# Optimization experiments

Hardware: AMD Instinct MI355X
Metric: run time of the kernel (lower is better)

## Reference

```python
import jax, jax.numpy as jnp
import numpy as np

TOP_K = 2


def setup_inputs() -> dict:
    key = jax.random.key(0)
    ks = jax.random.split(key, 8)
    B, S, H, I, E = 1, 1024, 2048, 1408, 8
    s = 0.02  # init scale for weights
    return {
        "hidden_states": jax.random.normal(ks[0], (B, S, H), jnp.float32),
        "gate_weight": jax.random.normal(ks[1], (E, H), jnp.float32) * s,
        "expert_gate_w": jax.random.normal(ks[2], (E, I, H), jnp.float32) * s,
        "expert_up_w": jax.random.normal(ks[3], (E, I, H), jnp.float32) * s,
        "expert_down_w": jax.random.normal(ks[4], (E, H, I), jnp.float32) * s,
        "shared_gate_w": jax.random.normal(ks[5], (I, H), jnp.float32) * s,
        "shared_up_w": jax.random.normal(ks[6], (I, H), jnp.float32) * s,
        "shared_down_w": jax.random.normal(ks[7], (H, I), jnp.float32) * s,
    }


def reference(hidden_states, gate_weight, expert_gate_w, expert_up_w, expert_down_w,
              shared_gate_w, shared_up_w, shared_down_w):
    B, S, H = hidden_states.shape
    E = gate_weight.shape[0]
    x = hidden_states.reshape(-1, H)          # [T, H]
    T = x.shape[0]

    # --- gate: top-k routing (e_score_correction_bias buffer is zeros -> no-op) ---
    logits = x @ gate_weight.T                # [T, E]
    topk_logits, topk_idx = jax.lax.top_k(logits, TOP_K)
    topk_w = jax.nn.softmax(topk_logits, axis=-1)  # [T, K]

    # per-token per-expert combine weight (0 for non-selected experts) [T, E]
    comb = jnp.zeros((T, E), x.dtype).at[jnp.arange(T)[:, None], topk_idx].add(topk_w)

    # --- routed experts: dense over E, weighted combine (mathematically identical
    # to the per-token loop since comb==0 for unselected experts) ---
    g = jnp.einsum('th,eih->tei', x, expert_gate_w)   # [T, E, I]
    u = jnp.einsum('th,eih->tei', x, expert_up_w)     # [T, E, I]
    h = jax.nn.silu(g) * u                            # [T, E, I]
    y = jnp.einsum('tei,ehi->teh', h, expert_down_w)  # [T, E, H]
    out = jnp.einsum('teh,te->th', y, comb)           # [T, H]

    # --- shared expert ---
    sh = (jax.nn.silu(x @ shared_gate_w.T) * (x @ shared_up_w.T)) @ shared_down_w.T
    out = out + sh
    return out.reshape(B, S, H)
```

## Files before the change

kernel.cpp:

```cpp
#include <hip/hip_runtime.h>
#include <hip/hip_bf16.h>

typedef unsigned short u16;
typedef __bf16 bf16x8 __attribute__((ext_vector_type(8)));
typedef float f32x4 __attribute__((ext_vector_type(4)));

#define H_DIM 2048
#define I_DIM 1408
#define T_TOK 1024
#define NEXP 8
#define LS 40

__device__ __forceinline__ u16 f2bf(float f) {
    union { float f; unsigned u; } v; v.f = f;
    unsigned r = v.u + 0x7FFFu + ((v.u >> 16) & 1u);
    return (u16)(r >> 16);
}
__device__ __forceinline__ unsigned pack2(float a, float b) {
    float2 t; t.x = a; t.y = b;
    __hip_bfloat162 h = __float22bfloat162_rn(t);
    union { __hip_bfloat162 h; unsigned u; } v; v.h = h;
    return v.u;
}
__device__ __forceinline__ uint2 pack4(float4 f) {
    uint2 r; r.x = pack2(f.x, f.y); r.y = pack2(f.z, f.w); return r;
}
__device__ __forceinline__ void g2l16(const void* g, void* l) {
    __builtin_amdgcn_global_load_lds((const __attribute__((address_space(1))) void*)g,
                                     (__attribute__((address_space(3))) void*)l, 16, 0, 0);
}

struct PrepArgs {
    const float* cin[6]; u16* cout[6]; int n16[6];
    const float* x; const float* gw; u16* xb;
    int* counts; int* tok; float* tw; unsigned* tslot;
};

__global__ __launch_bounds__(256)
void prep_kernel(PrepArgs a) {
    int z = blockIdx.z;
    if (z < 6) {
        int n = a.n16[z];
        const float4* in = (const float4*)a.cin[z];
        uint4* out = (uint4*)a.cout[z];
        for (int i = blockIdx.x * 256 + threadIdx.x; i < n; i += gridDim.x * 256) {
            const float4* p = in + (size_t)i * 4;
            float4 f0 = p[0], f1 = p[1], f2 = p[2], f3 = p[3];
            uint4 o0, o1;
            o0.x = pack2(f0.x, f0.y); o0.y = pack2(f0.z, f0.w);
            o0.z = pack2(f1.x, f1.y); o0.w = pack2(f1.z, f1.w);
            o1.x = pack2(f2.x, f2.y); o1.y = pack2(f2.z, f2.w);
            o1.z = pack2(f3.x, f3.y); o1.w = pack2(f3.z, f3.w);
            out[(size_t)i * 2]     = o0;
            out[(size_t)i * 2 + 1] = o1;
        }
    } else {
        if (blockIdx.x >= 256) return;
        int wave = threadIdx.x >> 6, lane = threadIdx.x & 63;
        int t = blockIdx.x * 4 + wave;
        const float4* xr = (const float4*)(a.x + (size_t)t * H_DIM);
        const float4* gw4 = (const float4*)a.gw;
        uint2* xbr = (uint2*)(a.xb + (size_t)t * H_DIM);
        float acc[NEXP];
#pragma unroll
        for (int e = 0; e < NEXP; e++) acc[e] = 0.f;
#pragma unroll
        for (int j = 0; j < 8; j++) {
            int c = lane + j * 64;
            float4 xv = xr[c];
            xbr[c] = pack4(xv);
#pragma unroll
            for (int e = 0; e < NEXP; e++) {
                float4 gv = gw4[e * 512 + c];
                acc[e] += xv.x * gv.x + xv.y * gv.y + xv.z * gv.z + xv.w * gv.w;
            }
        }
#pragma unroll
        for (int e = 0; e < NEXP; e++) {
#pragma unroll
            for (int off = 32; off > 0; off >>= 1) acc[e] += __shfl_xor(acc[e], off);
        }
        if (lane == 0) {
            int i0 = 0; float v0 = acc[0];
#pragma unroll
            for (int e = 1; e < NEXP; e++) if (acc[e] > v0) { v0 = acc[e]; i0 = e; }
            int i1 = -1; float v1 = -3.0e38f;
#pragma unroll
            for (int e = 0; e < NEXP; e++) if (e != i0 && acc[e] > v1) { v1 = acc[e]; i1 = e; }
            float ex = __expf(v1 - v0);
            float w0 = 1.f / (1.f + ex);
            float w1 = 1.f - w0;
            int s0 = atomicAdd(&a.counts[i0], 1);
            a.tok[i0 * T_TOK + s0] = t; a.tw[i0 * T_TOK + s0] = w0;
            a.tslot[t * 2] = ((unsigned)i0 << 16) | (unsigned)s0;
            int s1 = atomicAdd(&a.counts[i1], 1);
            a.tok[i1 * T_TOK + s1] = t; a.tw[i1 * T_TOK + s1] = w1;
            a.tslot[t * 2 + 1] = ((unsigned)i1 << 16) | (unsigned)s1;
        }
    }
}

__global__ __launch_bounds__(128, 2)
void gate_up_bf(const u16* __restrict__ xb,
                const u16* __restrict__ egb, const u16* __restrict__ eub,
                const u16* __restrict__ sgb, const u16* __restrict__ sub,
                const int* __restrict__ counts, const int* __restrict__ tok,
                const float* __restrict__ tw,
                u16* __restrict__ h_r, u16* __restrict__ h_s) {
    __shared__ u16 lA[64 * 64];
    __shared__ u16 lG[128 * 64];
    __shared__ u16 lU[128 * 64];

    int e = blockIdx.z;
    bool routed = (e < NEXP);
    int cnt, hbase; const u16 *Wg, *Wu; u16* hout;
    if (routed) {
        cnt = counts[e];
        int p = 0;
#pragma unroll
        for (int i = 0; i < NEXP; i++) { int c = counts[i]; if (i < e) p += c; }
        hbase = p;
        Wg = egb + (size_t)e * I_DIM * H_DIM;
        Wu = eub + (size_t)e * I_DIM * H_DIM;
        hout = h_r;
    } else { cnt = T_TOK; hbase = 0; Wg = sgb; Wu = sub; hout = h_s; }
    int m0 = blockIdx.y * 64;
    if (m0 >= cnt) return;
    int n0 = blockIdx.x * 128;

    int tid = threadIdx.x, lane = tid & 63, w = tid >> 6;
    int l3 = lane >> 3, cl = lane & 7;
    int cg = cl ^ l3;

    const u16* aptr[4];
#pragma unroll
    for (int j = 0; j < 4; j++) {
        int row = w * 32 + j * 8 + l3;
        int trow = m0 + row; if (trow > cnt - 1) trow = cnt - 1;
        int tix = routed ? tok[e * T_TOK + trow] : trow;
        aptr[j] = xb + (size_t)tix * H_DIM + cg * 8;
    }
    const u16* gbase = Wg + (size_t)(n0 + w * 64 + l3) * H_DIM + cg * 8;
    const u16* ubase = Wu + (size_t)(n0 + w * 64 + l3) * H_DIM + cg * 8;

    u16* aldsb = &lA[w * 2048];
    u16* gldsb = &lG[w * 4096];
    u16* uldsb = &lU[w * 4096];

    f32x4 zero = {0.f, 0.f, 0.f, 0.f};
    f32x4 accg[4][4], accu[4][4];
#pragma unroll
    for (int a = 0; a < 4; a++)
#pragma unroll
        for (int b = 0; b < 4; b++) { accg[a][b] = zero; accu[a][b] = zero; }

    int r16 = lane & 15, q = lane >> 4;

    for (int k0 = 0; k0 < H_DIM; k0 += 64) {
#pragma unroll
        for (int j = 0; j < 4; j++) g2l16(aptr[j] + k0, aldsb + j * 512);
#pragma unroll
        for (int j = 0; j < 8; j++) {
            g2l16(gbase + (size_t)j * 8 * H_DIM + k0, gldsb + j * 512);
            g2l16(ubase + (size_t)j * 8 * H_DIM + k0, uldsb + j * 512);
        }
        __syncthreads();
#pragma unroll
        for (int kh = 0; kh < 2; kh++) {
            bf16x8 af[4], gf[4], uf[4];
#pragma unroll
            for (int mi = 0; mi < 4; mi++) {
                int row = mi * 16 + r16;
                int ch = (kh * 4 + q) ^ (row & 7);
                af[mi] = *(const bf16x8*)&lA[row * 64 + ch * 8];
            }
#pragma unroll
            for (int ni = 0; ni < 4; ni++) {
                int row = w * 64 + ni * 16 + r16;
                int ch = (kh * 4 + q) ^ (row & 7);
                gf[ni] = *(const bf16x8*)&lG[row * 64 + ch * 8];
                uf[ni] = *(const bf16x8*)&lU[row * 64 + ch * 8];
            }
#pragma unroll
            for (int mi = 0; mi < 4; mi++)
#pragma unroll
                for (int ni = 0; ni < 4; ni++) {
                    accg[mi][ni] = __builtin_amdgcn_mfma_f32_16x16x32_bf16(af[mi], gf[ni], accg[mi][ni], 0, 0, 0);
                    accu[mi][ni] = __builtin_amdgcn_mfma_f32_16x16x32_bf16(af[mi], uf[ni], accu[mi][ni], 0, 0, 0);
                }
        }
        __syncthreads();
    }

#pragma unroll
    for (int mi = 0; mi < 4; mi++) {
#pragma unroll
        for (int r = 0; r < 4; r++) {
            int row = mi * 16 + q * 4 + r;
            int gr = m0 + row;
            if (gr < cnt) {
                float wt = routed ? tw[e * T_TOK + gr] : 1.0f;
                u16* hrow = hout + (size_t)(hbase + gr) * I_DIM + n0 + w * 64;
#pragma unroll
                for (int ni = 0; ni < 4; ni++) {
                    float g = accg[mi][ni][r], u = accu[mi][ni][r];
                    hrow[ni * 16 + r16] = f2bf((g / (1.f + __expf(-g))) * u * wt);
                }
            }
        }
    }
}

__global__ __launch_bounds__(128, 2)
void down_bf(const u16* __restrict__ h_r, const u16* __restrict__ h_s,
             const u16* __restrict__ edb, const u16* __restrict__ sdb,
             const int* __restrict__ counts, const int* __restrict__ tok,
             float* __restrict__ y_r, float* __restrict__ y_s) {
    __shared__ u16 lA[64 * 64];
    __shared__ u16 lB[128 * 64];

    int e = blockIdx.z;
    bool routed = (e < NEXP);
    int cnt, hbase; const u16* Wd; const u16* hin;
    if (routed) {
        cnt = counts[e];
        int p = 0;
#pragma unroll
        for (int i = 0; i < NEXP; i++) { int c = counts[i]; if (i < e) p += c; }
        hbase = p;
        Wd = edb + (size_t)e * H_DIM * I_DIM;
        hin = h_r;
    } else { cnt = T_TOK; hbase = 0; Wd = sdb; hin = h_s; }
    int m0 = blockIdx.y * 64;
    if (m0 >= cnt) return;
    int n0 = blockIdx.x * 128;

    int tid = threadIdx.x, lane = tid & 63, w = tid >> 6;
    int l3 = lane >> 3, cl = lane & 7;
    int cg = cl ^ l3;

    const u16* aptr[4];
#pragma unroll
    for (int j = 0; j < 4; j++) {
        int row = w * 32 + j * 8 + l3;
        int hr = m0 + row; if (hr > cnt - 1) hr = cnt - 1;
        aptr[j] = hin + (size_t)(hbase + hr) * I_DIM + cg * 8;
    }
    const u16* bbase = Wd + (size_t)(n0 + w * 64 + l3) * I_DIM + cg * 8;

    u16* aldsb = &lA[w * 2048];
    u16* bldsb = &lB[w * 4096];

    f32x4 zero = {0.f, 0.f, 0.f, 0.f};
    f32x4 acc[4][4];
#pragma unroll
    for (int a = 0; a < 4; a++)
#pragma unroll
        for (int b = 0; b < 4; b++) acc[a][b] = zero;

    int r16 = lane & 15, q = lane >> 4;

    for (int k0 = 0; k0 < I_DIM; k0 += 64) {
#pragma unroll
        for (int j = 0; j < 4; j++) g2l16(aptr[j] + k0, aldsb + j * 512);
#pragma unroll
        for (int j = 0; j < 8; j++) g2l16(bbase + (size_t)j * 8 * I_DIM + k0, bldsb + j * 512);
        __syncthreads();
#pragma unroll
        for (int kh = 0; kh < 2; kh++) {
            bf16x8 af[4], bfr[4];
#pragma unroll
            for (int mi = 0; mi < 4; mi++) {
                int row = mi * 16 + r16;
                int ch = (kh * 4 + q) ^ (row & 7);
                af[mi] = *(const bf16x8*)&lA[row * 64 + ch * 8];
            }
#pragma unroll
            for (int ni = 0; ni < 4; ni++) {
                int row = w * 64 + ni * 16 + r16;
                int ch = (kh * 4 + q) ^ (row & 7);
                bfr[ni] = *(const bf16x8*)&lB[row * 64 + ch * 8];
            }
#pragma unroll
            for (int mi = 0; mi < 4; mi++)
#pragma unroll
                for (int ni = 0; ni < 4; ni++)
                    acc[mi][ni] = __builtin_amdgcn_mfma_f32_16x16x32_bf16(af[mi], bfr[ni], acc[mi][ni], 0, 0, 0);
        }
        __syncthreads();
    }

#pragma unroll
    for (int mi = 0; mi < 4; mi++) {
#pragma unroll
        for (int r = 0; r < 4; r++) {
            int row = mi * 16 + q * 4 + r;
            int gr = m0 + row;
            if (gr < cnt) {
                float* yrow = (routed ? y_r + (size_t)(hbase + gr) * H_DIM
                                      : y_s + (size_t)gr * H_DIM) + n0 + w * 64;
#pragma unroll
                for (int ni = 0; ni < 4; ni++)
                    yrow[ni * 16 + r16] = acc[mi][ni][r];
            }
        }
    }
}

__global__ __launch_bounds__(256)
void reduce_kernel(const int* __restrict__ counts, const unsigned* __restrict__ tslot,
                   const float* __restrict__ y_r, const float* __restrict__ y_s,
                   float* __restrict__ out) {
    int t = blockIdx.x;
    int pre[NEXP]; int run = 0;
#pragma unroll
    for (int i = 0; i < NEXP; i++) { pre[i] = run; run += counts[i]; }
    unsigned t0 = tslot[t * 2], t1 = tslot[t * 2 + 1];
    int r0 = pre[t0 >> 16] + (int)(t0 & 0xffffu);
    int r1 = pre[t1 >> 16] + (int)(t1 & 0xffffu);
    const float4* ys = (const float4*)(y_s + (size_t)t * H_DIM);
    const float4* a0 = (const float4*)(y_r + (size_t)r0 * H_DIM);
    const float4* a1 = (const float4*)(y_r + (size_t)r1 * H_DIM);
    float4* o = (float4*)(out + (size_t)t * H_DIM);
#pragma unroll
    for (int j = 0; j < 2; j++) {
        int c = threadIdx.x + j * 256;
        float4 s = ys[c], b0 = a0[c], b1 = a1[c];
        float4 r;
        r.x = s.x + b0.x + b1.x; r.y = s.y + b0.y + b1.y;
        r.z = s.z + b0.z + b1.z; r.w = s.w + b0.w + b1.w;
        o[c] = r;
    }
}

__global__ __launch_bounds__(256)
void router_kernel(const float* __restrict__ x, const float* __restrict__ gw,
                   int* __restrict__ counts, int* __restrict__ tok, float* __restrict__ tw) {
    int wave = threadIdx.x >> 6;
    int lane = threadIdx.x & 63;
    int t = blockIdx.x * 4 + wave;
    const float* xr = x + (size_t)t * H_DIM;
    float acc[NEXP];
#pragma unroll
    for (int e = 0; e < NEXP; e++) acc[e] = 0.f;
    for (int h = lane; h < H_DIM; h += 64) {
        float xv = xr[h];
#pragma unroll
        for (int e = 0; e < NEXP; e++) acc[e] += xv * gw[e * H_DIM + h];
    }
#pragma unroll
    for (int e = 0; e < NEXP; e++) {
#pragma unroll
        for (int off = 32; off > 0; off >>= 1) acc[e] += __shfl_xor(acc[e], off);
    }
    if (lane == 0) {
        int i0 = 0; float v0 = acc[0];
#pragma unroll
        for (int e = 1; e < NEXP; e++) if (acc[e] > v0) { v0 = acc[e]; i0 = e; }
        int i1 = -1; float v1 = -3.0e38f;
#pragma unroll
        for (int e = 0; e < NEXP; e++) if (e != i0 && acc[e] > v1) { v1 = acc[e]; i1 = e; }
        float ex = __expf(v1 - v0);
        float w0 = 1.f / (1.f + ex);
        float w1 = 1.f - w0;
        int s0 = atomicAdd(&counts[i0], 1);
        tok[i0 * T_TOK + s0] = t; tw[i0 * T_TOK + s0] = w0;
        int s1 = atomicAdd(&counts[i1], 1);
        tok[i1 * T_TOK + s1] = t; tw[i1 * T_TOK + s1] = w1;
    }
}

__global__ __launch_bounds__(256, 2)
void gate_up_f32(const float* __restrict__ x,
                 const float* __restrict__ egw, const float* __restrict__ euw,
                 const float* __restrict__ sgw, const float* __restrict__ suw,
                 const int* __restrict__ counts, const int* __restrict__ tok,
                 const float* __restrict__ tw,
                 u16* __restrict__ h_r, u16* __restrict__ h_s) {
    __shared__ u16 lA[64 * LS];
    __shared__ u16 lG[128 * LS];
    __shared__ u16 lU[128 * LS];
    int e = blockIdx.z;
    bool routed = (e < NEXP);
    int cnt, hbase; const float *Wg, *Wu; u16* hout;
    if (routed) {
// ... 114 lines not shown
    int hr = m0 + arow; if (hr > cnt - 1) hr = cnt - 1;
    const u16* ap = hin + (size_t)(hbase + hr) * I_DIM + ac8 * 8;
    int sa = arow * LS + ac8 * 8;
    const float* bp[4]; int sb[4];
#pragma unroll
    for (int i = 0; i < 4; i++) {
        int slot = tid + i * 256;
        int row = slot >> 3, c4 = slot & 7;
        bp[i] = Wd + (size_t)(n0 + row) * I_DIM + c4 * 4;
        sb[i] = row * LS + c4 * 4;
    }
    f32x4 zero = {0.f, 0.f, 0.f, 0.f};
    f32x4 acc[4][2];
#pragma unroll
    for (int a = 0; a < 4; a++)
#pragma unroll
        for (int b = 0; b < 2; b++) acc[a][b] = zero;
    int r16 = lane & 15, kq = lane >> 4;
    uint4 ra = *(const uint4*)(ap);
    float4 rb[4];
#pragma unroll
    for (int i = 0; i < 4; i++) rb[i] = *(const float4*)(bp[i]);
    for (int k0 = 0; k0 < I_DIM; k0 += 32) {
        *(uint4*)&lA[sa] = ra;
#pragma unroll
        for (int i = 0; i < 4; i++) *(uint2*)&lB[sb[i]] = pack4(rb[i]);
        __syncthreads();
        if (k0 + 32 < I_DIM) {
            int kn = k0 + 32;
            ra = *(const uint4*)(ap + kn);
#pragma unroll
            for (int i = 0; i < 4; i++) rb[i] = *(const float4*)(bp[i] + kn);
        }
        bf16x8 af[4], bfr[2];
#pragma unroll
        for (int mi = 0; mi < 4; mi++) af[mi] = *(const bf16x8*)&lA[(mi * 16 + r16) * LS + kq * 8];
#pragma unroll
        for (int ni = 0; ni < 2; ni++) bfr[ni] = *(const bf16x8*)&lB[(w * 32 + ni * 16 + r16) * LS + kq * 8];
#pragma unroll
        for (int mi = 0; mi < 4; mi++)
#pragma unroll
            for (int ni = 0; ni < 2; ni++)
                acc[mi][ni] = __builtin_amdgcn_mfma_f32_16x16x32_bf16(af[mi], bfr[ni], acc[mi][ni], 0, 0, 0);
        __syncthreads();
    }
#pragma unroll
    for (int mi = 0; mi < 4; mi++) {
#pragma unroll
        for (int r = 0; r < 4; r++) {
            int row = mi * 16 + kq * 4 + r;
            int gr = m0 + row;
            if (gr < cnt) {
                int t = routed ? tok[e * T_TOK + gr] : gr;
                float* orow = out + (size_t)t * H_DIM + n0 + w * 32;
#pragma unroll
                for (int ni = 0; ni < 2; ni++)
                    atomicAdd(&orow[ni * 16 + r16], acc[mi][ni][r]);
            }
        }
    }
}

extern "C" void kernel_launch(void* const* d_in, const int* in_sizes, int n_in,
                              void* d_out, int out_size, void* d_ws, size_t ws_size,
                              hipStream_t stream) {
    const float* x   = (const float*)d_in[0];
    const float* gw  = (const float*)d_in[1];
    const float* egw = (const float*)d_in[2];
    const float* euw = (const float*)d_in[3];
    const float* edw = (const float*)d_in[4];
    const float* sgw = (const float*)d_in[5];
    const float* suw = (const float*)d_in[6];
    const float* sdw = (const float*)d_in[7];
    float* out = (float*)d_out;

    char* ws = (char*)d_ws;
    int*      counts = (int*)ws;
    int*      tok    = (int*)(ws + 256);
    float*    tw     = (float*)(ws + 33024);
    unsigned* tslot  = (unsigned*)(ws + 65792);
    u16*      h_r    = (u16*)(ws + 73984);
    u16*      h_s    = (u16*)(ws + 5841152);
    u16*      xb     = (u16*)(ws + 8724736);
    u16*      egb    = (u16*)(ws + 12919040);
    u16*      eub    = (u16*)(ws + 59056384);
    u16*      edb    = (u16*)(ws + 105193728);
    u16*      sgb    = (u16*)(ws + 151331072);
    u16*      sub    = (u16*)(ws + 157098240);
    u16*      sdb    = (u16*)(ws + 162865408);
    float*    y_r    = (float*)(ws + 12919040);
    float*    y_s    = (float*)(ws + 29696256);

    hipMemsetAsync(counts, 0, 32, stream);

    const size_t NEED = 168632576ull;
    if (ws_size >= NEED) {
        PrepArgs pa;
        pa.cin[0] = egw; pa.cout[0] = egb; pa.n16[0] = 1441792;
        pa.cin[1] = euw; pa.cout[1] = eub; pa.n16[1] = 1441792;
        pa.cin[2] = edw; pa.cout[2] = edb; pa.n16[2] = 1441792;
        pa.cin[3] = sgw; pa.cout[3] = sgb; pa.n16[3] = 180224;
        pa.cin[4] = suw; pa.cout[4] = sub; pa.n16[4] = 180224;
        pa.cin[5] = sdw; pa.cout[5] = sdb; pa.n16[5] = 180224;
        pa.x = x; pa.gw = gw; pa.xb = xb;
        pa.counts = counts; pa.tok = tok; pa.tw = tw; pa.tslot = tslot;
        prep_kernel<<<dim3(1024, 1, 7), 256, 0, stream>>>(pa);
        gate_up_bf<<<dim3(11, 16, 9), 128, 0, stream>>>(xb, egb, eub, sgb, sub, counts, tok, tw, h_r, h_s);
        down_bf<<<dim3(16, 16, 9), 128, 0, stream>>>(h_r, h_s, edb, sdb, counts, tok, y_r, y_s);
        reduce_kernel<<<1024, 256, 0, stream>>>(counts, tslot, y_r, y_s, out);
    } else {
        hipMemsetAsync(out, 0, (size_t)T_TOK * H_DIM * sizeof(float), stream);
        router_kernel<<<256, 256, 0, stream>>>(x, gw, counts, tok, tw);
        gate_up_f32<<<dim3(11, 16, 9), 256, 0, stream>>>(x, egw, euw, sgw, suw, counts, tok, tw, h_r, h_s);
        down_f32<<<dim3(16, 16, 9), 256, 0, stream>>>(h_r, h_s, edw, sdw, counts, tok, out);
    }
}
```

Before: 504.0 us.

## Overlap down-weight bf16 conversion with gate/up GEMM and use 4-wave blocks

The fp32-to-bf16 conversion of the down-projection weights moves out of the prep kernel into an extra z-slice of the gate/up GEMM launch, so it runs alongside the GEMM blocks. The prep kernel now converts only the gate/up weights, using a flat block mapping and batched loads. Both GEMM kernels switch from 2 waves to 4 waves per block with a 64x128 tile, so each wave now owns a 32-column slice, and launch bounds target 3 blocks per CU. This is meant to hide conversion bandwidth behind compute and raise occupancy, at the cost of fewer MFMAs per LDS fragment load.

```diff
diff --git a/kernel.cpp b/kernel.cpp
--- a/kernel.cpp
+++ b/kernel.cpp
@@ -30,34 +30,35 @@
                                      (__attribute__((address_space(3))) void*)l, 16, 0, 0);
 }
 
-struct PrepArgs {
-    const float* cin[6]; u16* cout[6]; int n16[6];
+struct Prep1Args {
+    const float* src[4]; u16* dst[4];
     const float* x; const float* gw; u16* xb;
     int* counts; int* tok; float* tw; unsigned* tslot;
 };
 
 __global__ __launch_bounds__(256)
-void prep_kernel(PrepArgs a) {
-    int z = blockIdx.z;
-    if (z < 6) {
-        int n = a.n16[z];
-        const float4* in = (const float4*)a.cin[z];
-        uint4* out = (uint4*)a.cout[z];
-        for (int i = blockIdx.x * 256 + threadIdx.x; i < n; i += gridDim.x * 256) {
-            const float4* p = in + (size_t)i * 4;
-            float4 f0 = p[0], f1 = p[1], f2 = p[2], f3 = p[3];
-            uint4 o0, o1;
-            o0.x = pack2(f0.x, f0.y); o0.y = pack2(f0.z, f0.w);
-            o0.z = pack2(f1.x, f1.y); o0.w = pack2(f1.z, f1.w);
-            o1.x = pack2(f2.x, f2.y); o1.y = pack2(f2.z, f2.w);
-            o1.z = pack2(f3.x, f3.y); o1.w = pack2(f3.z, f3.w);
-            out[(size_t)i * 2]     = o0;
-            out[(size_t)i * 2 + 1] = o1;
+void prep1_kernel(Prep1Args a) {
+    int b = blockIdx.x;
+    if (b < 1584) {
+        int r, rb;
+        if (b < 704)       { r = 0; rb = b; }
+        else if (b < 1408) { r = 1; rb = b - 704; }
+        else if (b < 1496) { r = 2; rb = b - 1408; }
+        else               { r = 3; rb = b - 1496; }
+        const float4* in = (const float4*)a.src[r];
+        uint2* out = (uint2*)a.dst[r];
+        size_t base = (size_t)rb * 8192 + threadIdx.x;
+#pragma unroll
+        for (int it = 0; it < 4; it++) {
+            float4 v[8];
+#pragma unroll
+            for (int j = 0; j < 8; j++) v[j] = in[base + it * 2048 + j * 256];
+#pragma unroll
+            for (int j = 0; j < 8; j++) out[base + it * 2048 + j * 256] = pack4(v[j]);
         }
     } else {
-        if (blockIdx.x >= 256) return;
         int wave = threadIdx.x >> 6, lane = threadIdx.x & 63;
-        int t = blockIdx.x * 4 + wave;
+        int t = (b - 1584) * 4 + wave;
         const float4* xr = (const float4*)(a.x + (size_t)t * H_DIM);
         const float4* gw4 = (const float4*)a.gw;
         uint2* xbr = (uint2*)(a.xb + (size_t)t * H_DIM);
@@ -100,18 +101,46 @@
     }
 }
 
-__global__ __launch_bounds__(128, 2)
+#define EDW_F4 5767168
+__global__ __launch_bounds__(256, 3)
 void gate_up_bf(const u16* __restrict__ xb,
                 const u16* __restrict__ egb, const u16* __restrict__ eub,
                 const u16* __restrict__ sgb, const u16* __restrict__ sub,
                 const int* __restrict__ counts, const int* __restrict__ tok,
                 const float* __restrict__ tw,
-                u16* __restrict__ h_r, u16* __restrict__ h_s) {
+                u16* __restrict__ h_r, u16* __restrict__ h_s,
+                const float* __restrict__ edw_f, const float* __restrict__ sdw_f,
+                u16* __restrict__ edb, u16* __restrict__ sdb) {
+    int e = blockIdx.z;
+    if (e == 9) {
+        int b = blockIdx.y * 11 + blockIdx.x;
+        size_t base = (size_t)b * 36864 + threadIdx.x;
+        const float4* ein = (const float4*)edw_f;
+        const float4* sin_ = (const float4*)sdw_f;
+        uint2* eout = (uint2*)edb;
+        uint2* sout = (uint2*)sdb;
+        for (int it = 0; it < 18; it++) {
+            size_t g0 = base + (size_t)it * 2048;
+            float4 v[8];
+#pragma unroll
+            for (int j = 0; j < 8; j++) {
+                size_t g = g0 + j * 256;
+                v[j] = (g < EDW_F4) ? ein[g] : sin_[g - EDW_F4];
+            }
+#pragma unroll
+            for (int j = 0; j < 8; j++) {
+                size_t g = g0 + j * 256;
+                if (g < EDW_F4) eout[g] = pack4(v[j]);
+                else            sout[g - EDW_F4] = pack4(v[j]);
+            }
+        }
+        return;
+    }
+
     __shared__ u16 lA[64 * 64];
     __shared__ u16 lG[128 * 64];
     __shared__ u16 lU[128 * 64];
 
-    int e = blockIdx.z;
     bool routed = (e < NEXP);
     int cnt, hbase; const u16 *Wg, *Wu; u16* hout;
     if (routed) {
@@ -129,45 +158,48 @@
     int n0 = blockIdx.x * 128;
 
     int tid = threadIdx.x, lane = tid & 63, w = tid >> 6;
-    int l3 = lane >> 3, cl = lane & 7;
-    int cg = cl ^ l3;
-
-    const u16* aptr[4];
-#pragma unroll
-    for (int j = 0; j < 4; j++) {
-        int row = w * 32 + j * 8 + l3;
+
+    const u16* aptr[2]; u16* alds[2];
+#pragma unroll
+    for (int j = 0; j < 2; j++) {
+        int chunk = w * 128 + j * 64 + lane;
+        int row = chunk >> 3, cl = chunk & 7;
+        int cg = cl ^ (row & 7);
         int trow = m0 + row; if (trow > cnt - 1) trow = cnt - 1;
         int tix = routed ? tok[e * T_TOK + trow] : trow;
         aptr[j] = xb + (size_t)tix * H_DIM + cg * 8;
-    }
-    const u16* gbase = Wg + (size_t)(n0 + w * 64 + l3) * H_DIM + cg * 8;
-    const u16* ubase = Wu + (size_t)(n0 + w * 64 + l3) * H_DIM + cg * 8;
-
-    u16* aldsb = &lA[w * 2048];
-    u16* gldsb = &lG[w * 4096];
-    u16* uldsb = &lU[w * 4096];
+        alds[j] = &lA[(w * 128 + j * 64) * 8];
+    }
+    const u16* gptr[4]; const u16* uptr[4]; u16* glds[4]; u16* ulds[4];
+#pragma unroll
+    for (int j = 0; j < 4; j++) {
+        int chunk = w * 256 + j * 64 + lane;
+        int row = chunk >> 3, cl = chunk & 7;
+        int cg = cl ^ (row & 7);
+        gptr[j] = Wg + (size_t)(n0 + row) * H_DIM + cg * 8;
+        uptr[j] = Wu + (size_t)(n0 + row) * H_DIM + cg * 8;
+        glds[j] = &lG[(w * 256 + j * 64) * 8];
+        ulds[j] = &lU[(w * 256 + j * 64) * 8];
+    }
 
     f32x4 zero = {0.f, 0.f, 0.f, 0.f};
-    f32x4 accg[4][4], accu[4][4];
+    f32x4 accg[4][2], accu[4][2];
 #pragma unroll
     for (int a = 0; a < 4; a++)
 #pragma unroll
-        for (int b = 0; b < 4; b++) { accg[a][b] = zero; accu[a][b] = zero; }
+        for (int b = 0; b < 2; b++) { accg[a][b] = zero; accu[a][b] = zero; }
 
     int r16 = lane & 15, q = lane >> 4;
 
     for (int k0 = 0; k0 < H_DIM; k0 += 64) {
 #pragma unroll
-        for (int j = 0; j < 4; j++) g2l16(aptr[j] + k0, aldsb + j * 512);
-#pragma unroll
-        for (int j = 0; j < 8; j++) {
-            g2l16(gbase + (size_t)j * 8 * H_DIM + k0, gldsb + j * 512);
-            g2l16(ubase + (size_t)j * 8 * H_DIM + k0, uldsb + j * 512);
-        }
+        for (int j = 0; j < 2; j++) g2l16(aptr[j] + k0, alds[j]);
+#pragma unroll
+        for (int j = 0; j < 4; j++) { g2l16(gptr[j] + k0, glds[j]); g2l16(uptr[j] + k0, ulds[j]); }
         __syncthreads();
 #pragma unroll
         for (int kh = 0; kh < 2; kh++) {
-            bf16x8 af[4], gf[4], uf[4];
+            bf16x8 af[4], gf[2], uf[2];
 #pragma unroll
             for (int mi = 0; mi < 4; mi++) {
                 int row = mi * 16 + r16;
@@ -175,8 +207,8 @@
                 af[mi] = *(const bf16x8*)&lA[row * 64 + ch * 8];
             }
 #pragma unroll
-            for (int ni = 0; ni < 4; ni++) {
-                int row = w * 64 + ni * 16 + r16;
+            for (int ni = 0; ni < 2; ni++) {
+                int row = w * 32 + ni * 16 + r16;
                 int ch = (kh * 4 + q) ^ (row & 7);
                 gf[ni] = *(const bf16x8*)&lG[row * 64 + ch * 8];
                 uf[ni] = *(const bf16x8*)&lU[row * 64 + ch * 8];
@@ -184,7 +216,7 @@
 #pragma unroll
             for (int mi = 0; mi < 4; mi++)
 #pragma unroll
-                for (int ni = 0; ni < 4; ni++) {
+                for (int ni = 0; ni < 2; ni++) {
                     accg[mi][ni] = __builtin_amdgcn_mfma_f32_16x16x32_bf16(af[mi], gf[ni], accg[mi][ni], 0, 0, 0);
                     accu[mi][ni] = __builtin_amdgcn_mfma_f32_16x16x32_bf16(af[mi], uf[ni], accu[mi][ni], 0, 0, 0);
                 }
@@ -200,9 +232,9 @@
             int gr = m0 + row;
             if (gr < cnt) {
                 float wt = routed ? tw[e * T_TOK + gr] : 1.0f;
-                u16* hrow = hout + (size_t)(hbase + gr) * I_DIM + n0 + w * 64;
-#pragma unroll
-                for (int ni = 0; ni < 4; ni++) {
+                u16* hrow = hout + (size_t)(hbase + gr) * I_DIM + n0 + w * 32;
+#pragma unroll
+                for (int ni = 0; ni < 2; ni++) {
                     float g = accg[mi][ni][r], u = accu[mi][ni][r];
                     hrow[ni * 16 + r16] = f2bf((g / (1.f + __expf(-g))) * u * wt);
                 }
@@ -211,7 +243,7 @@
     }
 }
 
-__global__ __launch_bounds__(128, 2)
+__global__ __launch_bounds__(256, 3)
 void down_bf(const u16* __restrict__ h_r, const u16* __restrict__ h_s,
              const u16* __restrict__ edb, const u16* __restrict__ sdb,
              const int* __restrict__ counts, const int* __restrict__ tok,
@@ -236,39 +268,45 @@
     int n0 = blockIdx.x * 128;
 
     int tid = threadIdx.x, lane = tid & 63, w = tid >> 6;
-    int l3 = lane >> 3, cl = lane & 7;
-    int cg = cl ^ l3;
-
-    const u16* aptr[4];
-#pragma unroll
-    for (int j = 0; j < 4; j++) {
-        int row = w * 32 + j * 8 + l3;
+
+    const u16* aptr[2]; u16* alds[2];
+#pragma unroll
+    for (int j = 0; j < 2; j++) {
+        int chunk = w * 128 + j * 64 + lane;
+        int row = chunk >> 3, cl = chunk & 7;
+        int cg = cl ^ (row & 7);
         int hr = m0 + row; if (hr > cnt - 1) hr = cnt - 1;
         aptr[j] = hin + (size_t)(hbase + hr) * I_DIM + cg * 8;
-    }
-    const u16* bbase = Wd + (size_t)(n0 + w * 64 + l3) * I_DIM + cg * 8;
-
-    u16* aldsb = &lA[w * 2048];
-    u16* bldsb = &lB[w * 4096];
+        alds[j] = &lA[(w * 128 + j * 64) * 8];
+    }
+    const u16* bptr[4]; u16* blds[4];
+#pragma unroll
+    for (int j = 0; j < 4; j++) {
+        int chunk = w * 256 + j * 64 + lane;
+        int row = chunk >> 3, cl = chunk & 7;
+        int cg = cl ^ (row & 7);
+        bptr[j] = Wd + (size_t)(n0 + row) * I_DIM + cg * 8;
+        blds[j] = &lB[(w * 256 + j * 64) * 8];
+    }
 
     f32x4 zero = {0.f, 0.f, 0.f, 0.f};
-    f32x4 acc[4][4];
+    f32x4 acc[4][2];
 #pragma unroll
     for (int a = 0; a < 4; a++)
 #pragma unroll
-        for (int b = 0; b < 4; b++) acc[a][b] = zero;
+        for (int b = 0; b < 2; b++) acc[a][b] = zero;
 
     int r16 = lane & 15, q = lane >> 4;
 
     for (int k0 = 0; k0 < I_DIM; k0 += 64) {
 #pragma unroll
-        for (int j = 0; j < 4; j++) g2l16(aptr[j] + k0, aldsb + j * 512);
-#pragma unroll
-        for (int j = 0; j < 8; j++) g2l16(bbase + (size_t)j * 8 * I_DIM + k0, bldsb + j * 512);
+        for (int j = 0; j < 2; j++) g2l16(aptr[j] + k0, alds[j]);
+#pragma unroll
+        for (int j = 0; j < 4; j++) g2l16(bptr[j] + k0, blds[j]);
         __syncthreads();
 #pragma unroll
         for (int kh = 0; kh < 2; kh++) {
-            bf16x8 af[4], bfr[4];
+            bf16x8 af[4], bfr[2];
 #pragma unroll
             for (int mi = 0; mi < 4; mi++) {
                 int row = mi * 16 + r16;
@@ -276,15 +314,15 @@
                 af[mi] = *(const bf16x8*)&lA[row * 64 + ch * 8];
             }
 #pragma unroll
-            for (int ni = 0; ni < 4; ni++) {
-                int row = w * 64 + ni * 16 + r16;
+            for (int ni = 0; ni < 2; ni++) {
+                int row = w * 32 + ni * 16 + r16;
                 int ch = (kh * 4 + q) ^ (row & 7);
                 bfr[ni] = *(const bf16x8*)&lB[row * 64 + ch * 8];
             }
 #pragma unroll
             for (int mi = 0; mi < 4; mi++)
 #pragma unroll
-                for (int ni = 0; ni < 4; ni++)
+                for (int ni = 0; ni < 2; ni++)
                     acc[mi][ni] = __builtin_amdgcn_mfma_f32_16x16x32_bf16(af[mi], bfr[ni], acc[mi][ni], 0, 0, 0);
         }
         __syncthreads();
@@ -298,9 +336,9 @@
             int gr = m0 + row;
             if (gr < cnt) {
                 float* yrow = (routed ? y_r + (size_t)(hbase + gr) * H_DIM
-                                      : y_s + (size_t)gr * H_DIM) + n0 + w * 64;
-#pragma unroll
-                for (int ni = 0; ni < 4; ni++)
+                                      : y_s + (size_t)gr * H_DIM) + n0 + w * 32;
+#pragma unroll
+                for (int ni = 0; ni < 2; ni++)
                     yrow[ni * 16 + r16] = acc[mi][ni][r];
             }
         }
@@ -594,18 +632,17 @@
 
     const size_t NEED = 168632576ull;
     if (ws_size >= NEED) {
-        PrepArgs pa;
-        pa.cin[0] = egw; pa.cout[0] = egb; pa.n16[0] = 1441792;
-        pa.cin[1] = euw; pa.cout[1] = eub; pa.n16[1] = 1441792;
-        pa.cin[2] = edw; pa.cout[2] = edb; pa.n16[2] = 1441792;
-        pa.cin[3] = sgw; pa.cout[3] = sgb; pa.n16[3] = 180224;
-        pa.cin[4] = suw; pa.cout[4] = sub; pa.n16[4] = 180224;
-        pa.cin[5] = sdw; pa.cout[5] = sdb; pa.n16[5] = 180224;
+        Prep1Args pa;
+        pa.src[0] = egw; pa.dst[0] = egb;
+        pa.src[1] = euw; pa.dst[1] = eub;
+        pa.src[2] = sgw; pa.dst[2] = sgb;
+        pa.src[3] = suw; pa.dst[3] = sub;
         pa.x = x; pa.gw = gw; pa.xb = xb;
         pa.counts = counts; pa.tok = tok; pa.tw = tw; pa.tslot = tslot;
-        prep_kernel<<<dim3(1024, 1, 7), 256, 0, stream>>>(pa);
-        gate_up_bf<<<dim3(11, 16, 9), 128, 0, stream>>>(xb, egb, eub, sgb, sub, counts, tok, tw, h_r, h_s);
-        down_bf<<<dim3(16, 16, 9), 128, 0, stream>>>(h_r, h_s, edb, sdb, counts, tok, y_r, y_s);
+        prep1_kernel<<<1840, 256, 0, stream>>>(pa);
+        gate_up_bf<<<dim3(11, 16, 10), 256, 0, stream>>>(xb, egb, eub, sgb, sub, counts, tok, tw,
+                                                         h_r, h_s, edw, sdw, edb, sdb);
+        down_bf<<<dim3(16, 16, 9), 256, 0, stream>>>(h_r, h_s, edb, sdb, counts, tok, y_r, y_s);
         reduce_kernel<<<1024, 256, 0, stream>>>(counts, tslot, y_r, y_s, out);
     } else {
         hipMemsetAsync(out, 0, (size_t)T_TOK * H_DIM * sizeof(float), stream);
```

After: 476.6 us. -5.4%, faster.

## Convert fp32 expert weights to bf16 inside GEMM tiles, drop prep conversion pass

Applied to the files above, without the earlier changes.

Removes the separate weight-conversion kernel that read all fp32 expert weights and wrote bf16 copies each call. The GEMMs now stream the fp32 weights straight into LDS and convert them to bf16 while loading fragments. The blocks are reshaped to 256 threads with a smaller N per wave, and the flattened 1D grid interleaves M tiles so blocks sharing a weight tile run close together for L2 reuse. The trade-off is twice the LDS and global bytes per weight tile inside the GEMM and extra conversion ALU work in the inner loop, in exchange for skipping a full read and write pass over the weights.

```diff
diff --git a/kernel.cpp b/kernel.cpp
--- a/kernel.cpp
+++ b/kernel.cpp
@@ -25,149 +25,256 @@
 __device__ __forceinline__ uint2 pack4(float4 f) {
     uint2 r; r.x = pack2(f.x, f.y); r.y = pack2(f.z, f.w); return r;
 }
+__device__ __forceinline__ bf16x8 cvt8(f32x4 a, f32x4 b) {
+    union { uint4 u; bf16x8 v; } r;
+    r.u.x = pack2(a[0], a[1]); r.u.y = pack2(a[2], a[3]);
+    r.u.z = pack2(b[0], b[1]); r.u.w = pack2(b[2], b[3]);
+    return r.v;
+}
 __device__ __forceinline__ void g2l16(const void* g, void* l) {
     __builtin_amdgcn_global_load_lds((const __attribute__((address_space(1))) void*)g,
                                      (__attribute__((address_space(3))) void*)l, 16, 0, 0);
 }
 
-struct PrepArgs {
-    const float* cin[6]; u16* cout[6]; int n16[6];
-    const float* x; const float* gw; u16* xb;
-    int* counts; int* tok; float* tw; unsigned* tslot;
-};
-
 __global__ __launch_bounds__(256)
-void prep_kernel(PrepArgs a) {
-    int z = blockIdx.z;
-    if (z < 6) {
-        int n = a.n16[z];
-        const float4* in = (const float4*)a.cin[z];
-        uint4* out = (uint4*)a.cout[z];
-        for (int i = blockIdx.x * 256 + threadIdx.x; i < n; i += gridDim.x * 256) {
-            const float4* p = in + (size_t)i * 4;
-            float4 f0 = p[0], f1 = p[1], f2 = p[2], f3 = p[3];
-            uint4 o0, o1;
-            o0.x = pack2(f0.x, f0.y); o0.y = pack2(f0.z, f0.w);
-            o0.z = pack2(f1.x, f1.y); o0.w = pack2(f1.z, f1.w);
-            o1.x = pack2(f2.x, f2.y); o1.y = pack2(f2.z, f2.w);
-            o1.z = pack2(f3.x, f3.y); o1.w = pack2(f3.z, f3.w);
-            out[(size_t)i * 2]     = o0;
-            out[(size_t)i * 2 + 1] = o1;
-        }
-    } else {
-        if (blockIdx.x >= 256) return;
-        int wave = threadIdx.x >> 6, lane = threadIdx.x & 63;
-        int t = blockIdx.x * 4 + wave;
-        const float4* xr = (const float4*)(a.x + (size_t)t * H_DIM);
-        const float4* gw4 = (const float4*)a.gw;
-        uint2* xbr = (uint2*)(a.xb + (size_t)t * H_DIM);
-        float acc[NEXP];
-#pragma unroll
-        for (int e = 0; e < NEXP; e++) acc[e] = 0.f;
-#pragma unroll
-        for (int j = 0; j < 8; j++) {
-            int c = lane + j * 64;
-            float4 xv = xr[c];
-            xbr[c] = pack4(xv);
-#pragma unroll
-            for (int e = 0; e < NEXP; e++) {
-                float4 gv = gw4[e * 512 + c];
-                acc[e] += xv.x * gv.x + xv.y * gv.y + xv.z * gv.z + xv.w * gv.w;
-            }
-        }
+void router_x_kernel(const float* __restrict__ x, const float* __restrict__ gw,
+                     u16* __restrict__ xb,
+                     int* __restrict__ counts, int* __restrict__ tok,
+                     float* __restrict__ tw, unsigned* __restrict__ tslot) {
+    int wave = threadIdx.x >> 6, lane = threadIdx.x & 63;
+    int t = blockIdx.x * 4 + wave;
+    const float4* xr = (const float4*)(x + (size_t)t * H_DIM);
+    const float4* gw4 = (const float4*)gw;
+    uint2* xbr = (uint2*)(xb + (size_t)t * H_DIM);
+    float acc[NEXP];
+#pragma unroll
+    for (int e = 0; e < NEXP; e++) acc[e] = 0.f;
+#pragma unroll
+    for (int j = 0; j < 8; j++) {
+        int c = lane + j * 64;
+        float4 xv = xr[c];
+        xbr[c] = pack4(xv);
 #pragma unroll
         for (int e = 0; e < NEXP; e++) {
-#pragma unroll
-            for (int off = 32; off > 0; off >>= 1) acc[e] += __shfl_xor(acc[e], off);
-        }
-        if (lane == 0) {
-            int i0 = 0; float v0 = acc[0];
-#pragma unroll
-            for (int e = 1; e < NEXP; e++) if (acc[e] > v0) { v0 = acc[e]; i0 = e; }
-            int i1 = -1; float v1 = -3.0e38f;
-#pragma unroll
-            for (int e = 0; e < NEXP; e++) if (e != i0 && acc[e] > v1) { v1 = acc[e]; i1 = e; }
-            float ex = __expf(v1 - v0);
-            float w0 = 1.f / (1.f + ex);
-            float w1 = 1.f - w0;
-            int s0 = atomicAdd(&a.counts[i0], 1);
-            a.tok[i0 * T_TOK + s0] = t; a.tw[i0 * T_TOK + s0] = w0;
-            a.tslot[t * 2] = ((unsigned)i0 << 16) | (unsigned)s0;
-            int s1 = atomicAdd(&a.counts[i1], 1);
-            a.tok[i1 * T_TOK + s1] = t; a.tw[i1 * T_TOK + s1] = w1;
-            a.tslot[t * 2 + 1] = ((unsigned)i1 << 16) | (unsigned)s1;
-        }
-    }
-}
-
-__global__ __launch_bounds__(128, 2)
-void gate_up_bf(const u16* __restrict__ xb,
-                const u16* __restrict__ egb, const u16* __restrict__ eub,
-                const u16* __restrict__ sgb, const u16* __restrict__ sub,
+            float4 gv = gw4[e * 512 + c];
+            acc[e] += xv.x * gv.x + xv.y * gv.y + xv.z * gv.z + xv.w * gv.w;
+        }
+    }
+#pragma unroll
+    for (int e = 0; e < NEXP; e++) {
+#pragma unroll
+        for (int off = 32; off > 0; off >>= 1) acc[e] += __shfl_xor(acc[e], off);
+    }
+    if (lane == 0) {
+        int i0 = 0; float v0 = acc[0];
+#pragma unroll
+        for (int e = 1; e < NEXP; e++) if (acc[e] > v0) { v0 = acc[e]; i0 = e; }
+        int i1 = -1; float v1 = -3.0e38f;
+#pragma unroll
+        for (int e = 0; e < NEXP; e++) if (e != i0 && acc[e] > v1) { v1 = acc[e]; i1 = e; }
+        float ex = __expf(v1 - v0);
+        float w0 = 1.f / (1.f + ex);
+        float w1 = 1.f - w0;
+        int s0 = atomicAdd(&counts[i0], 1);
+        tok[i0 * T_TOK + s0] = t; tw[i0 * T_TOK + s0] = w0;
+        tslot[t * 2] = ((unsigned)i0 << 16) | (unsigned)s0;
+        int s1 = atomicAdd(&counts[i1], 1);
+        tok[i1 * T_TOK + s1] = t; tw[i1 * T_TOK + s1] = w1;
+        tslot[t * 2 + 1] = ((unsigned)i1 << 16) | (unsigned)s1;
+    }
+}
+
+__global__ __launch_bounds__(256, 3)
+void gate_up_fd(const u16* __restrict__ xb,
+                const float* __restrict__ egw, const float* __restrict__ euw,
+                const float* __restrict__ sgw, const float* __restrict__ suw,
                 const int* __restrict__ counts, const int* __restrict__ tok,
                 const float* __restrict__ tw,
                 u16* __restrict__ h_r, u16* __restrict__ h_s) {
-    __shared__ u16 lA[64 * 64];
-    __shared__ u16 lG[128 * 64];
-    __shared__ u16 lU[128 * 64];
-
-    int e = blockIdx.z;
-    bool routed = (e < NEXP);
-    int cnt, hbase; const u16 *Wg, *Wu; u16* hout;
+    __shared__ u16  lA[64 * 32];
+    __shared__ float lG[128 * 32];
+    __shared__ float lU[128 * 32];
+
+    int i = blockIdx.x;
+    int m_lo = (i >> 3) & 3;
+    int group = ((i >> 5) << 3) | (i & 7);
+    if (group >= 396) return;
+    int eq = group / 44;
+    int rem = group - eq * 44;
+    int n0 = (rem >> 2) * 128;
+    int m = (rem & 3) * 4 + m_lo;
+
+    bool routed = (eq < NEXP);
+    int cnt, hbase; const float *Wg, *Wu; u16* hout;
     if (routed) {
-        cnt = counts[e];
+        cnt = counts[eq];
         int p = 0;
 #pragma unroll
-        for (int i = 0; i < NEXP; i++) { int c = counts[i]; if (i < e) p += c; }
+        for (int ii = 0; ii < NEXP; ii++) { int c = counts[ii]; if (ii < eq) p += c; }
         hbase = p;
-        Wg = egb + (size_t)e * I_DIM * H_DIM;
-        Wu = eub + (size_t)e * I_DIM * H_DIM;
+        Wg = egw + (size_t)eq * I_DIM * H_DIM;
+        Wu = euw + (size_t)eq * I_DIM * H_DIM;
         hout = h_r;
-    } else { cnt = T_TOK; hbase = 0; Wg = sgb; Wu = sub; hout = h_s; }
-    int m0 = blockIdx.y * 64;
+    } else { cnt = T_TOK; hbase = 0; Wg = sgw; Wu = suw; hout = h_s; }
+    int m0 = m * 64;
     if (m0 >= cnt) return;
-    int n0 = blockIdx.x * 128;
 
     int tid = threadIdx.x, lane = tid & 63, w = tid >> 6;
-    int l3 = lane >> 3, cl = lane & 7;
-    int cg = cl ^ l3;
-
-    const u16* aptr[4];
+
+    int La = w * 64 + lane;
+    int arow = La >> 2;
+    int agc = (La & 3) ^ (arow & 3);
+    int trow = m0 + arow; if (trow > cnt - 1) trow = cnt - 1;
+    int tix = routed ? tok[eq * T_TOK + trow] : trow;
+    const u16* aptr = xb + (size_t)tix * H_DIM + agc * 8;
+    u16* adst = &lA[(w * 64) * 8];
+
+    const float* gptr[4]; const float* uptr[4]; float* gdst[4]; float* udst[4];
 #pragma unroll
     for (int j = 0; j < 4; j++) {
-        int row = w * 32 + j * 8 + l3;
-        int trow = m0 + row; if (trow > cnt - 1) trow = cnt - 1;
-        int tix = routed ? tok[e * T_TOK + trow] : trow;
-        aptr[j] = xb + (size_t)tix * H_DIM + cg * 8;
-    }
-    const u16* gbase = Wg + (size_t)(n0 + w * 64 + l3) * H_DIM + cg * 8;
-    const u16* ubase = Wu + (size_t)(n0 + w * 64 + l3) * H_DIM + cg * 8;
-
-    u16* aldsb = &lA[w * 2048];
-    u16* gldsb = &lG[w * 4096];
-    u16* uldsb = &lU[w * 4096];
+        int L = w * 256 + j * 64 + lane;
+        int row = L >> 3;
+        int gc = (L & 7) ^ ((row & 3) << 1);
+        gptr[j] = Wg + (size_t)(n0 + row) * H_DIM + gc * 4;
+        uptr[j] = Wu + (size_t)(n0 + row) * H_DIM + gc * 4;
+        gdst[j] = &lG[(w * 256 + j * 64) * 4];
+        udst[j] = &lU[(w * 256 + j * 64) * 4];
+    }
 
     f32x4 zero = {0.f, 0.f, 0.f, 0.f};
-    f32x4 accg[4][4], accu[4][4];
+    f32x4 accg[4][2], accu[4][2];
 #pragma unroll
     for (int a = 0; a < 4; a++)
 #pragma unroll
-        for (int b = 0; b < 4; b++) { accg[a][b] = zero; accu[a][b] = zero; }
+        for (int b = 0; b < 2; b++) { accg[a][b] = zero; accu[a][b] = zero; }
 
     int r16 = lane & 15, q = lane >> 4;
-
-    for (int k0 = 0; k0 < H_DIM; k0 += 64) {
-#pragma unroll
-        for (int j = 0; j < 4; j++) g2l16(aptr[j] + k0, aldsb + j * 512);
-#pragma unroll
-        for (int j = 0; j < 8; j++) {
-            g2l16(gbase + (size_t)j * 8 * H_DIM + k0, gldsb + j * 512);
-            g2l16(ubase + (size_t)j * 8 * H_DIM + k0, uldsb + j * 512);
-        }
+    int offa[4], offg[2];
+#pragma unroll
+    for (int mi = 0; mi < 4; mi++) {
+        int row = mi * 16 + r16;
+        offa[mi] = row * 32 + (q ^ (row & 3)) * 8;
+    }
+#pragma unroll
+    for (int ni = 0; ni < 2; ni++) {
+        int row = w * 32 + ni * 16 + r16;
+        offg[ni] = row * 32 + ((2 * q) ^ ((row & 3) << 1)) * 4;
+    }
+
+    for (int k0 = 0; k0 < H_DIM; k0 += 32) {
+        g2l16(aptr + k0, adst);
+#pragma unroll
+        for (int j = 0; j < 4; j++) { g2l16(gptr[j] + k0, gdst[j]); g2l16(uptr[j] + k0, udst[j]); }
+        __syncthreads();
+        bf16x8 af[4], gf[2], uf[2];
+#pragma unroll
+        for (int mi = 0; mi < 4; mi++) af[mi] = *(const bf16x8*)&lA[offa[mi]];
+#pragma unroll
+        for (int ni = 0; ni < 2; ni++) {
+            const f32x4* pg = (const f32x4*)&lG[offg[ni]];
+            gf[ni] = cvt8(pg[0], pg[1]);
+            const f32x4* pu = (const f32x4*)&lU[offg[ni]];
+            uf[ni] = cvt8(pu[0], pu[1]);
+        }
+#pragma unroll
+        for (int mi = 0; mi < 4; mi++)
+#pragma unroll
+            for (int ni = 0; ni < 2; ni++) {
+                accg[mi][ni] = __builtin_amdgcn_mfma_f32_16x16x32_bf16(af[mi], gf[ni], accg[mi][ni], 0, 0, 0);
+                accu[mi][ni] = __builtin_amdgcn_mfma_f32_16x16x32_bf16(af[mi], uf[ni], accu[mi][ni], 0, 0, 0);
+            }
+        __syncthreads();
+    }
+
+#pragma unroll
+    for (int mi = 0; mi < 4; mi++) {
+#pragma unroll
+        for (int r = 0; r < 4; r++) {
+            int row = mi * 16 + q * 4 + r;
+            int gr = m0 + row;
+            if (gr < cnt) {
+                float wt = routed ? tw[eq * T_TOK + gr] : 1.0f;
+                u16* hrow = hout + (size_t)(hbase + gr) * I_DIM + n0 + w * 32;
+#pragma unroll
+                for (int ni = 0; ni < 2; ni++) {
+                    float g = accg[mi][ni][r], u = accu[mi][ni][r];
+                    hrow[ni * 16 + r16] = f2bf((g / (1.f + __expf(-g))) * u * wt);
+                }
+            }
+        }
+    }
+}
+
+__global__ __launch_bounds__(256, 3)
+void down_fd(const u16* __restrict__ h_r, const u16* __restrict__ h_s,
+             const float* __restrict__ edw, const float* __restrict__ sdw,
+             const int* __restrict__ counts, const int* __restrict__ tok,
+             float* __restrict__ y_r, float* __restrict__ y_s) {
+    __shared__ u16  lA[64 * 64];
+    __shared__ float lB[128 * 64];
+
+    int i = blockIdx.x;
+    int m_lo = (i >> 3) & 3;
+    int group = ((i >> 5) << 3) | (i & 7);
+    int eq = group >> 6;
+    int rem = group & 63;
+    int n0 = (rem >> 2) * 128;
+    int m = (rem & 3) * 4 + m_lo;
+
+    bool routed = (eq < NEXP);
+    int cnt, hbase; const float* Wd; const u16* hin;
+    if (routed) {
+        cnt = counts[eq];
+        int p = 0;
+#pragma unroll
+        for (int ii = 0; ii < NEXP; ii++) { int c = counts[ii]; if (ii < eq) p += c; }
+        hbase = p;
+        Wd = edw + (size_t)eq * H_DIM * I_DIM;
+        hin = h_r;
+    } else { cnt = T_TOK; hbase = 0; Wd = sdw; hin = h_s; }
+    int m0 = m * 64;
+    if (m0 >= cnt) return;
+
+    int tid = threadIdx.x, lane = tid & 63, w = tid >> 6;
+
+    const u16* aptr[2]; u16* adst[2];
+#pragma unroll
+    for (int j = 0; j < 2; j++) {
+        int L = w * 128 + j * 64 + lane;
+        int row = L >> 3;
+        int gc = (L & 7) ^ (row & 7);
+        int hr = m0 + row; if (hr > cnt - 1) hr = cnt - 1;
+        aptr[j] = hin + (size_t)(hbase + hr) * I_DIM + gc * 8;
+        adst[j] = &lA[(w * 128 + j * 64) * 8];
+    }
+    const float* bptr[8]; float* bdst[8];
+#pragma unroll
+    for (int j = 0; j < 8; j++) {
+        int L = w * 512 + j * 64 + lane;
+        int row = L >> 4;
+        int gc = (L & 15) ^ ((row & 7) << 1);
+        bptr[j] = Wd + (size_t)(n0 + row) * I_DIM + gc * 4;
+        bdst[j] = &lB[(w * 512 + j * 64) * 4];
+    }
+
+    f32x4 zero = {0.f, 0.f, 0.f, 0.f};
+    f32x4 acc[4][2];
+#pragma unroll
+    for (int a = 0; a < 4; a++)
+#pragma unroll
+        for (int b = 0; b < 2; b++) acc[a][b] = zero;
+
+    int r16 = lane & 15, q = lane >> 4;
+
+    for (int k0 = 0; k0 < I_DIM; k0 += 64) {
+#pragma unroll
+        for (int j = 0; j < 2; j++) g2l16(aptr[j] + k0, adst[j]);
+#pragma unroll
+        for (int j = 0; j < 8; j++) g2l16(bptr[j] + k0, bdst[j]);
         __syncthreads();
 #pragma unroll
         for (int kh = 0; kh < 2; kh++) {
-            bf16x8 af[4], gf[4], uf[4];
+            bf16x8 af[4], bfr[2];
 #pragma unroll
             for (int mi = 0; mi < 4; mi++) {
                 int row = mi * 16 + r16;
@@ -175,116 +282,16 @@
                 af[mi] = *(const bf16x8*)&lA[row * 64 + ch * 8];
             }
 #pragma unroll
-            for (int ni = 0; ni < 4; ni++) {
-                int row = w * 64 + ni * 16 + r16;
-                int ch = (kh * 4 + q) ^ (row & 7);
-                gf[ni] = *(const bf16x8*)&lG[row * 64 + ch * 8];
-                uf[ni] = *(const bf16x8*)&lU[row * 64 + ch * 8];
+            for (int ni = 0; ni < 2; ni++) {
+                int row = w * 32 + ni * 16 + r16;
+                int ch = (2 * (kh * 4 + q)) ^ ((row & 7) << 1);
+                const f32x4* pb = (const f32x4*)&lB[row * 64 + ch * 4];
+                bfr[ni] = cvt8(pb[0], pb[1]);
             }
 #pragma unroll
             for (int mi = 0; mi < 4; mi++)
 #pragma unroll
-                for (int ni = 0; ni < 4; ni++) {
-                    accg[mi][ni] = __builtin_amdgcn_mfma_f32_16x16x32_bf16(af[mi], gf[ni], accg[mi][ni], 0, 0, 0);
-                    accu[mi][ni] = __builtin_amdgcn_mfma_f32_16x16x32_bf16(af[mi], uf[ni], accu[mi][ni], 0, 0, 0);
-                }
-        }
-        __syncthreads();
-    }
-
-#pragma unroll
-    for (int mi = 0; mi < 4; mi++) {
-#pragma unroll
-        for (int r = 0; r < 4; r++) {
-            int row = mi * 16 + q * 4 + r;
-            int gr = m0 + row;
-            if (gr < cnt) {
-                float wt = routed ? tw[e * T_TOK + gr] : 1.0f;
-                u16* hrow = hout + (size_t)(hbase + gr) * I_DIM + n0 + w * 64;
-#pragma unroll
-                for (int ni = 0; ni < 4; ni++) {
-                    float g = accg[mi][ni][r], u = accu[mi][ni][r];
-                    hrow[ni * 16 + r16] = f2bf((g / (1.f + __expf(-g))) * u * wt);
-                }
-            }
-        }
-    }
-}
-
-__global__ __launch_bounds__(128, 2)
-void down_bf(const u16* __restrict__ h_r, const u16* __restrict__ h_s,
-             const u16* __restrict__ edb, const u16* __restrict__ sdb,
-             const int* __restrict__ counts, const int* __restrict__ tok,
-             float* __restrict__ y_r, float* __restrict__ y_s) {
-    __shared__ u16 lA[64 * 64];
-    __shared__ u16 lB[128 * 64];
-
-    int e = blockIdx.z;
-    bool routed = (e < NEXP);
-    int cnt, hbase; const u16* Wd; const u16* hin;
-    if (routed) {
-        cnt = counts[e];
-        int p = 0;
-#pragma unroll
-        for (int i = 0; i < NEXP; i++) { int c = counts[i]; if (i < e) p += c; }
-        hbase = p;
-        Wd = edb + (size_t)e * H_DIM * I_DIM;
-        hin = h_r;
-    } else { cnt = T_TOK; hbase = 0; Wd = sdb; hin = h_s; }
-    int m0 = blockIdx.y * 64;
-    if (m0 >= cnt) return;
-    int n0 = blockIdx.x * 128;
-
-    int tid = threadIdx.x, lane = tid & 63, w = tid >> 6;
-    int l3 = lane >> 3, cl = lane & 7;
-    int cg = cl ^ l3;
-
-    const u16* aptr[4];
-#pragma unroll
-    for (int j = 0; j < 4; j++) {
-        int row = w * 32 + j * 8 + l3;
-        int hr = m0 + row; if (hr > cnt - 1) hr = cnt - 1;
-        aptr[j] = hin + (size_t)(hbase + hr) * I_DIM + cg * 8;
-    }
-    const u16* bbase = Wd + (size_t)(n0 + w * 64 + l3) * I_DIM + cg * 8;
-
-    u16* aldsb = &lA[w * 2048];
-    u16* bldsb = &lB[w * 4096];
-
-    f32x4 zero = {0.f, 0.f, 0.f, 0.f};
-    f32x4 acc[4][4];
-#pragma unroll
-    for (int a = 0; a < 4; a++)
-#pragma unroll
-        for (int b = 0; b < 4; b++) acc[a][b] = zero;
-
-    int r16 = lane & 15, q = lane >> 4;
-
-    for (int k0 = 0; k0 < I_DIM; k0 += 64) {
-#pragma unroll
-        for (int j = 0; j < 4; j++) g2l16(aptr[j] + k0, aldsb + j * 512);
-#pragma unroll
-        for (int j = 0; j < 8; j++) g2l16(bbase + (size_t)j * 8 * I_DIM + k0, bldsb + j * 512);
-        __syncthreads();
-#pragma unroll
-        for (int kh = 0; kh < 2; kh++) {
-            bf16x8 af[4], bfr[4];
-#pragma unroll
-            for (int mi = 0; mi < 4; mi++) {
-                int row = mi * 16 + r16;
-                int ch = (kh * 4 + q) ^ (row & 7);
-                af[mi] = *(const bf16x8*)&lA[row * 64 + ch * 8];
-            }
-#pragma unroll
-            for (int ni = 0; ni < 4; ni++) {
-                int row = w * 64 + ni * 16 + r16;
-                int ch = (kh * 4 + q) ^ (row & 7);
-                bfr[ni] = *(const bf16x8*)&lB[row * 64 + ch * 8];
-            }
-#pragma unroll
-            for (int mi = 0; mi < 4; mi++)
-#pragma unroll
-                for (int ni = 0; ni < 4; ni++)
+                for (int ni = 0; ni < 2; ni++)
                     acc[mi][ni] = __builtin_amdgcn_mfma_f32_16x16x32_bf16(af[mi], bfr[ni], acc[mi][ni], 0, 0, 0);
         }
         __syncthreads();
@@ -298,9 +305,9 @@
             int gr = m0 + row;
             if (gr < cnt) {
                 float* yrow = (routed ? y_r + (size_t)(hbase + gr) * H_DIM
-                                      : y_s + (size_t)gr * H_DIM) + n0 + w * 64;
-#pragma unroll
-                for (int ni = 0; ni < 4; ni++)
+                                      : y_s + (size_t)gr * H_DIM) + n0 + w * 32;
+#pragma unroll
+                for (int ni = 0; ni < 2; ni++)
                     yrow[ni * 16 + r16] = acc[mi][ni][r];
             }
         }
@@ -581,31 +588,16 @@
     u16*      h_r    = (u16*)(ws + 73984);
     u16*      h_s    = (u16*)(ws + 5841152);
     u16*      xb     = (u16*)(ws + 8724736);
-    u16*      egb    = (u16*)(ws + 12919040);
-    u16*      eub    = (u16*)(ws + 59056384);
-    u16*      edb    = (u16*)(ws + 105193728);
-    u16*      sgb    = (u16*)(ws + 151331072);
-    u16*      sub    = (u16*)(ws + 157098240);
-    u16*      sdb    = (u16*)(ws + 162865408);
     float*    y_r    = (float*)(ws + 12919040);
     float*    y_s    = (float*)(ws + 29696256);
 
     hipMemsetAsync(counts, 0, 32, stream);
 
-    const size_t NEED = 168632576ull;
+    const size_t NEED = 38084864ull;
     if (ws_size >= NEED) {
-        PrepArgs pa;
-        pa.cin[0] = egw; pa.cout[0] = egb; pa.n16[0] = 1441792;
-        pa.cin[1] = euw; pa.cout[1] = eub; pa.n16[1] = 1441792;
-        pa.cin[2] = edw; pa.cout[2] = edb; pa.n16[2] = 1441792;
-        pa.cin[3] = sgw; pa.cout[3] = sgb; pa.n16[3] = 180224;
-        pa.cin[4] = suw; pa.cout[4] = sub; pa.n16[4] = 180224;
-        pa.cin[5] = sdw; pa.cout[5] = sdb; pa.n16[5] = 180224;
-        pa.x = x; pa.gw = gw; pa.xb = xb;
-        pa.counts = counts; pa.tok = tok; pa.tw = tw; pa.tslot = tslot;
-        prep_kernel<<<dim3(1024, 1, 7), 256, 0, stream>>>(pa);
-        gate_up_bf<<<dim3(11, 16, 9), 128, 0, stream>>>(xb, egb, eub, sgb, sub, counts, tok, tw, h_r, h_s);
-        down_bf<<<dim3(16, 16, 9), 128, 0, stream>>>(h_r, h_s, edb, sdb, counts, tok, y_r, y_s);
+        router_x_kernel<<<256, 256, 0, stream>>>(x, gw, xb, counts, tok, tw, tslot);
+        gate_up_fd<<<1600, 256, 0, stream>>>(xb, egw, euw, sgw, suw, counts, tok, tw, h_r, h_s);
+        down_fd<<<2304, 256, 0, stream>>>(h_r, h_s, edw, sdw, counts, tok, y_r, y_s);
         reduce_kernel<<<1024, 256, 0, stream>>>(counts, tslot, y_r, y_s, out);
     } else {
         hipMemsetAsync(out, 0, (size_t)T_TOK * H_DIM * sizeof(float), stream);
```

After: 672.3 us. 33.4% more time.
